# Kernel optimization log

Measured on AMD Instinct MI355X. Metric: run time of the kernel, lower is better.

## Reference

```python
import jax, jax.numpy as jnp
import numpy as np


def _make_grid(h, w, stride=1):
    """Vectorized port of gen_grid_coordinates_exp. Returns (1, 3*Ho, 3*Wo, 2) float32,
    last dim = (x_norm, y_norm) in [-1,1] (torch grid_sample convention)."""
    rows = np.arange(0, h, stride)
    cols = np.arange(0, w, stride)
    theta = -((rows + 0.5) / h * np.pi - np.pi / 2)          # (Ho,)
    phi = (cols + 0.5) / w * 2 * np.pi - np.pi               # (Wo,)
    dtheta = np.pi / h
    dphi = 2 * np.pi / w
    # 3x3 tangent-plane offsets (du: horizontal, dv: vertical), per get_exp_duv
    du = np.tan(dphi) * np.array([[-1., 0., 1.]] * 3)                      # (3,3)
    dv = np.tan(dtheta) * np.array([[1., 1., 1.], [0., 0., 0.], [-1., -1., -1.]])
    T = theta[:, None, None, None]   # (Ho,1,1,1)
    P = phi[None, :, None, None]     # (1,Wo,1,1)
    u_x = -du * np.sin(P) - dv * np.sin(T) * np.cos(P)       # (Ho,Wo,3,3)
    u_y = du * np.cos(P) - dv * np.sin(T) * np.sin(P)
    u_z = dv * np.cos(T) + np.zeros_like(u_x)
    u_norm = np.sqrt(u_x ** 2 + u_y ** 2 + u_z ** 2)
    u_div = np.where(u_norm == 0, 1.0, u_norm)
    c, s = np.cos(u_norm), np.sin(u_norm)
    ex = np.cos(T) * np.cos(P) * c + u_x / u_div * s
    ey = np.cos(T) * np.sin(P) * c + u_y / u_div * s
    ez = np.sin(T) * c + u_z / u_div * s
    new_phi = np.arctan2(ey, ex)
    new_theta = np.arcsin(np.clip(ez, -1.0, 1.0))
    new_r = (-new_theta + np.pi / 2) * h / np.pi - 0.5
    new_c = ((new_phi + np.pi) * w / (2 * np.pi) - 0.5 + w) % w
    # kernel center samples the original integer pixel exactly
    new_r[:, :, 1, 1] = rows[:, None]
    new_c[:, :, 1, 1] = cols[None, :]
    gx = new_c * 2.0 / w - 1.0
    gy = new_r * 2.0 / h - 1.0
    grid = np.stack([gx, gy], axis=-1)                        # (Ho,Wo,3,3,2)
    Ho, Wo = len(rows), len(cols)
    grid = grid.transpose(0, 2, 1, 3, 4).reshape(1, Ho * 3, Wo * 3, 2)
    return grid.astype(np.float32)


def _grid_sample_bilinear(x, grid):
    """torch.nn.functional.grid_sample(mode='bilinear', padding='zeros', align_corners=False).
    x: (B,C,H,W); grid: (1,Hg,Wg,2) shared across batch."""
    B, C, H, W = x.shape
    gx = grid[0, ..., 0]
    gy = grid[0, ..., 1]
    Hg, Wg = gx.shape
    ix = ((gx + 1.0) * W - 1.0) * 0.5   # unnormalize, align_corners=False
    iy = ((gy + 1.0) * H - 1.0) * 0.5
    x0 = jnp.floor(ix); x1 = x0 + 1.0
    y0 = jnp.floor(iy); y1 = y0 + 1.0
    xf = x.reshape(B, C, H * W)

    def corner(xc, yc, wgt):
        valid = (xc >= 0) & (xc < W) & (yc >= 0) & (yc < H)
        xi = jnp.clip(xc, 0, W - 1).astype(jnp.int32)
        yi = jnp.clip(yc, 0, H - 1).astype(jnp.int32)
        idx = (yi * W + xi).reshape(-1)                      # (Hg*Wg,)
        w_eff = (wgt * valid.astype(wgt.dtype)).reshape(-1)  # zero-pad OOB
        return xf[:, :, idx] * w_eff                          # (B,C,Hg*Wg)

    out = (corner(x0, y0, (x1 - ix) * (y1 - iy))
           + corner(x1, y0, (ix - x0) * (y1 - iy))
           + corner(x0, y1, (x1 - ix) * (iy - y0))
           + corner(x1, y1, (ix - x0) * (iy - y0)))
    return out.reshape(B, C, Hg, Wg)


def setup_inputs() -> dict:
    key = jax.random.key(0)
    k1, k2 = jax.random.split(key)
    B, Cin, Cout, H, W = 4, 128, 256, 128, 256
    x = jax.random.normal(k1, (B, Cin, H, W), dtype=jnp.float32)
    # kaiming_uniform_(a=sqrt(5)) -> U(-1/sqrt(fan_in), 1/sqrt(fan_in)), fan_in = Cin*9
    bound = 1.0 / np.sqrt(Cin * 9)
    weight = jax.random.uniform(k2, (Cout, Cin, 3, 3), dtype=jnp.float32,
                                minval=-bound, maxval=bound)
    bias = jnp.zeros((Cout,), dtype=jnp.float32)
    grid = jnp.asarray(_make_grid(H, W, stride=1))  # (1, 3H, 3W, 2)
    return {"x": x, "weight": weight, "bias": bias, "grid": grid}


def reference(x, weight, bias, grid):
    sampled = _grid_sample_bilinear(x, grid)                 # (B,C,3H,3W)
    out = jax.lax.conv_general_dilated(
        sampled, weight, window_strides=(3, 3), padding='VALID',
        dimension_numbers=('NCHW', 'OIHW', 'NCHW'))          # (B,Cout,H,W)
    return out + bias[None, :, None, None]
```

## Files before the change

kernel.cpp:

```cpp
#include <hip/hip_runtime.h>


#define Hh   128
#define Ww   256
#define HWp  (Hh*Ww)
#define CIN  128
#define COUT 256
#define KTOT 1152
#define NPTS (384*768)
#define BM   128
#define BN   256
#define BK   32
#define NKS  (KTOT/BK)

typedef __attribute__((ext_vector_type(8))) __bf16 bf16x8;
typedef __attribute__((ext_vector_type(4))) float  f32x4;

__global__ void build_table(const float* __restrict__ grid,
                            int2* __restrict__ tI, float4* __restrict__ tW) {
    int g = blockIdx.x * 256 + threadIdx.x;
    if (g >= NPTS) return;
    int hh = g / 768, ww = g - hh * 768;
    int ho = hh / 3, ii = hh - 3 * ho;
    int wo = ww / 3, jj = ww - 3 * wo;

    float gx = grid[2 * g + 0];
    float gy = grid[2 * g + 1];
    float ix = ((gx + 1.0f) * (float)Ww - 1.0f) * 0.5f;
    float iy = ((gy + 1.0f) * (float)Hh - 1.0f) * 0.5f;
    float x0f = floorf(ix), y0f = floorf(iy);
    int x0 = (int)x0f, y0 = (int)y0f;
    float wx1 = ix - x0f, wx0 = 1.0f - wx1;
    float wy1 = iy - y0f, wy0 = 1.0f - wy1;

    float wyt = (y0 >= 0 && y0 < Hh) ? wy0 : 0.0f;
    float wyb = (y0 + 1 >= 0 && y0 + 1 < Hh) ? wy1 : 0.0f;
    int r0 = min(max(y0, 0), Hh - 1);
    int r1 = min(max(y0 + 1, 0), Hh - 1);

    int xb; float cw0, cw1;
    if (x0 < 0)            { xb = 0;      cw0 = wx1; cw1 = 0.0f; }
    else if (x0 > Ww - 2)  { xb = Ww - 2; cw0 = 0.0f; cw1 = wx0; }
    else                   { xb = x0;     cw0 = wx0; cw1 = wx1; }

    int e = (ho * Ww + wo) * 9 + ii * 3 + jj;
    tI[e] = make_int2(r0 * Ww + xb, r1 * Ww + xb);
    tW[e] = make_float4(cw0 * wyt, cw1 * wyt, cw0 * wyb, cw1 * wyb);
}

__global__ void conv_w(const float* __restrict__ w, __bf16* __restrict__ wt) {
    int o = blockIdx.x * 256 + threadIdx.x;
    if (o >= NKS * COUT * BK) return;
    int kk = o & (BK - 1);
    int n  = (o >> 5) & (COUT - 1);
    int ks = o >> 13;
    wt[o] = (__bf16)w[n * KTOT + ks * BK + kk];
}

__global__ __launch_bounds__(512, 2) void sphconv_gemm(
    const float* __restrict__ x, const __bf16* __restrict__ wt,
    const float* __restrict__ bias, const int2* __restrict__ tI,
    const float4* __restrict__ tW, float* __restrict__ out) {

    __shared__ int2   sTI[BM * 9];
    __shared__ float4 sTW[BM * 9];
    __shared__ __align__(16) __bf16 sA[BM * 40];
    __shared__ __align__(16) __bf16 sB[BN * 40];

    const int t   = threadIdx.x;
    const int m0  = blockIdx.x * BM;
    const int b   = m0 >> 15;
    const int sp0 = m0 & (HWp - 1);
    const float* xb_ = x + (size_t)b * (CIN * HWp);

    for (int e = t; e < BM * 9; e += 512) {
        sTI[e] = tI[sp0 * 9 + e];
        sTW[e] = tW[sp0 * 9 + e];
    }

    const int lane = t & 63;
    const int wid  = t >> 6;
    const int wrow = wid >> 2;
    const int wcol = wid & 3;
    const int quad = lane >> 4;
    const int l16  = lane & 15;

    const int mr_s = t & 127;
    const int kg   = t >> 7;

    f32x4 acc[4][4];
#pragma unroll
    for (int r = 0; r < 4; ++r)
#pragma unroll
        for (int c = 0; c < 4; ++c) {
            f32x4 z = {0.0f, 0.0f, 0.0f, 0.0f};
            acc[r][c] = z;
        }

    __syncthreads();

    for (int ks = 0; ks < NKS; ++ks) {
        int k  = ks * BK + kg * 8;
        int ci = k / 9;
        int ij = k - ci * 9;
        const float* img = xb_ + ci * HWp;
        bf16x8 av;
#pragma unroll
        for (int j = 0; j < 8; ++j) {
            int2   o  = sTI[mr_s * 9 + ij];
            float4 wv = sTW[mr_s * 9 + ij];
            float a0 = img[o.x], a1 = img[o.x + 1];
            float b0 = img[o.y], b1 = img[o.y + 1];
            float v = a0 * wv.x + a1 * wv.y + b0 * wv.z + b1 * wv.w;
            av[j] = (__bf16)v;
            if (++ij == 9) { ij = 0; img += HWp; }
        }
        *(bf16x8*)(&sA[mr_s * 40 + kg * 8]) = av;

        {
            const __bf16* src = wt + ks * (COUT * BK) + t * 16;
            bf16x8 v0 = *(const bf16x8*)(src);
            bf16x8 v1 = *(const bf16x8*)(src + 8);
            int n  = t >> 1;
            int kq = (t & 1) * 16;
            *(bf16x8*)(&sB[n * 40 + kq])     = v0;
            *(bf16x8*)(&sB[n * 40 + kq + 8]) = v1;
        }
        __syncthreads();

        bf16x8 af[4], bfr[4];
#pragma unroll
        for (int r = 0; r < 4; ++r)
            af[r] = *(const bf16x8*)(&sA[(wrow * 64 + r * 16 + l16) * 40 + quad * 8]);
#pragma unroll
        for (int c = 0; c < 4; ++c)
            bfr[c] = *(const bf16x8*)(&sB[(wcol * 64 + c * 16 + l16) * 40 + quad * 8]);
#pragma unroll
        for (int r = 0; r < 4; ++r)
#pragma unroll
            for (int c = 0; c < 4; ++c)
                acc[r][c] = __builtin_amdgcn_mfma_f32_16x16x32_bf16(
                    af[r], bfr[c], acc[r][c], 0, 0, 0);
        __syncthreads();
    }

#pragma unroll
    for (int c = 0; c < 4; ++c) {
        int n = wcol * 64 + c * 16 + l16;
        float bv = bias[n];
        float* outn = out + (((size_t)(b * COUT + n)) << 15) + sp0;
#pragma unroll
        for (int r = 0; r < 4; ++r) {
            int mbase = wrow * 64 + r * 16 + quad * 4;
#pragma unroll
            for (int i = 0; i < 4; ++i)
                outn[mbase + i] = acc[r][c][i] + bv;
        }
    }
}

extern "C" void kernel_launch(void* const* d_in, const int* in_sizes, int n_in,
                              void* d_out, int out_size, void* d_ws, size_t ws_size,
                              hipStream_t stream) {
    const float* x    = (const float*)d_in[0];
    const float* w    = (const float*)d_in[1];
    const float* bias = (const float*)d_in[2];
    const float* grid = (const float*)d_in[3];
    float* out = (float*)d_out;

    char* ws = (char*)d_ws;
    int2*   tI = (int2*)(ws);
    float4* tW = (float4*)(ws + 2359296);
    __bf16* wt = (__bf16*)(ws + 7077888);

    build_table<<<(NPTS + 255) / 256, 256, 0, stream>>>(grid, tI, tW);
    conv_w<<<(NKS * COUT * BK + 255) / 256, 256, 0, stream>>>(w, wt);
    sphconv_gemm<<<(4 * HWp) / BM, 512, 0, stream>>>(x, wt, bias, tI, tW, out);
}
```

Baseline: 414.3 us.

## Reorder GEMM K dimension tap-major to hoist gather table lookups

Reorders the reduction index from channel-major (ci*9+tap) to tap-major (tap*128+ci) in both the weight repack kernel and the GEMM. Each thread now reads its gather offsets and bilinear weights from shared memory once per K-step instead of once per element. It also removes the per-element division and wrap logic, and uses float2 loads for the adjacent pixel pairs. Output stores are widened to float4, and launch bounds are raised to four blocks per CU, which caps registers hard enough that the 64-float accumulator may spill.

```diff
diff --git a/kernel.cpp b/kernel.cpp
--- a/kernel.cpp
+++ b/kernel.cpp
@@ -54,10 +54,13 @@
     int kk = o & (BK - 1);
     int n  = (o >> 5) & (COUT - 1);
     int ks = o >> 13;
-    wt[o] = (__bf16)w[n * KTOT + ks * BK + kk];
+    int kp = ks * BK + kk;
+    int ij = kp >> 7;
+    int ci = kp & (CIN - 1);
+    wt[o] = (__bf16)w[n * KTOT + ci * 9 + ij];
 }
 
-__global__ __launch_bounds__(512, 2) void sphconv_gemm(
+__global__ __launch_bounds__(512, 4) void sphconv_gemm(
     const float* __restrict__ x, const __bf16* __restrict__ wt,
     const float* __restrict__ bias, const int2* __restrict__ tI,
     const float4* __restrict__ tW, float* __restrict__ out) {
@@ -100,20 +103,18 @@
     __syncthreads();
 
     for (int ks = 0; ks < NKS; ++ks) {
-        int k  = ks * BK + kg * 8;
-        int ci = k / 9;
-        int ij = k - ci * 9;
-        const float* img = xb_ + ci * HWp;
+        const int ij  = ks >> 2;
+        const int ci0 = (ks & 3) * 32 + kg * 8;
+        const int2   o  = sTI[mr_s * 9 + ij];
+        const float4 wv = sTW[mr_s * 9 + ij];
+        const float* img = xb_ + (size_t)ci0 * HWp;
         bf16x8 av;
 #pragma unroll
         for (int j = 0; j < 8; ++j) {
-            int2   o  = sTI[mr_s * 9 + ij];
-            float4 wv = sTW[mr_s * 9 + ij];
-            float a0 = img[o.x], a1 = img[o.x + 1];
-            float b0 = img[o.y], b1 = img[o.y + 1];
-            float v = a0 * wv.x + a1 * wv.y + b0 * wv.z + b1 * wv.w;
-            av[j] = (__bf16)v;
-            if (++ij == 9) { ij = 0; img += HWp; }
+            float2 p0 = *(const float2*)(img + o.x);
+            float2 p1 = *(const float2*)(img + o.y);
+            av[j] = (__bf16)(p0.x * wv.x + p0.y * wv.y + p1.x * wv.z + p1.y * wv.w);
+            img += HWp;
         }
         *(bf16x8*)(&sA[mr_s * 40 + kg * 8]) = av;
 
@@ -152,9 +153,9 @@
 #pragma unroll
         for (int r = 0; r < 4; ++r) {
             int mbase = wrow * 64 + r * 16 + quad * 4;
-#pragma unroll
-            for (int i = 0; i < 4; ++i)
-                outn[mbase + i] = acc[r][c][i] + bv;
+            float4 v = make_float4(acc[r][c][0] + bv, acc[r][c][1] + bv,
+                                   acc[r][c][2] + bv, acc[r][c][3] + bv);
+            *(float4*)(&outn[mbase]) = v;
         }
     }
 }
```

After: 393.5 us. -5.0%, faster.
